# Kernel optimization log

Hardware: AMD Instinct MI355X
Metric: run time of the kernel (lower is better)

Reference implementation:

```python
import jax, jax.numpy as jnp
import numpy as np

LN_EPS = 1e-5

def _layernorm(x, gamma, beta):
    mu = jnp.mean(x, axis=-1, keepdims=True)
    var = jnp.mean(jnp.square(x - mu), axis=-1, keepdims=True)
    return (x - mu) * jax.lax.rsqrt(var + LN_EPS) * gamma + beta

def _gcn_layer(A_hat, H, W, b, g, beta):
    # batched dense-equivalent of per-batch torch.sparse.mm: (B,N,N)@(B,N,F)
    H = jnp.einsum('bnm,bmf->bnf', A_hat, H)
    H = H @ W + b            # Linear
    H = _layernorm(H, g, beta)
    return jax.nn.relu(H)    # dropout is identity in eval

def setup_inputs() -> dict:
    key = jax.random.key(0)
    ks = jax.random.split(key, 8)
    B, N, F, Hd, K, G = 16, 2048, 64, 256, 128, 18
    fuse = Hd + G  # 274
    return {
        'A_hat': jax.random.uniform(ks[0], (B, N, N), dtype=jnp.float32),
        'X': jax.random.normal(ks[1], (B, N, F), dtype=jnp.float32),
        'global_vec': jax.random.normal(ks[2], (B, G), dtype=jnp.float32),
        'W1': jax.random.normal(ks[3], (F, Hd), dtype=jnp.float32) / np.sqrt(F),
        'b1': jnp.zeros((Hd,), jnp.float32),
        'g1': jnp.ones((Hd,), jnp.float32),
        'beta1': jnp.zeros((Hd,), jnp.float32),
        'W2': jax.random.normal(ks[4], (Hd, Hd), dtype=jnp.float32) / np.sqrt(Hd),
        'b2': jnp.zeros((Hd,), jnp.float32),
        'g2': jnp.ones((Hd,), jnp.float32),
        'beta2': jnp.zeros((Hd,), jnp.float32),
        'Ws': jax.random.normal(ks[5], (fuse, 1), dtype=jnp.float32) / np.sqrt(fuse),
        'bs': jnp.zeros((1,), jnp.float32),
        'Wa': jax.random.normal(ks[6], (fuse, K), dtype=jnp.float32) / np.sqrt(fuse),
        'ba': jnp.zeros((K,), jnp.float32),
    }

def reference(A_hat, X, global_vec, W1, b1, g1, beta1, W2, b2, g2, beta2, Ws, bs, Wa, ba):
    H = _gcn_layer(A_hat, X, W1, b1, g1, beta1)
    H = _gcn_layer(A_hat, H, W2, b2, g2, beta2)
    gcnout = jnp.mean(H, axis=1)                       # 'mean' readout -> (B, hidden)
    fused = jnp.concatenate([gcnout, global_vec], axis=-1)  # (B, hidden+18)
    pred_y_reg = (fused @ Ws + bs)[:, 0]               # (B,)
    pred_arr_reg = fused @ Wa + ba                     # (B, K)
    return pred_y_reg, pred_arr_reg
```

## Files before the change

### kernel.cpp

```cpp
#include <hip/hip_runtime.h>

typedef unsigned short u16;
typedef __attribute__((ext_vector_type(8))) short bf16x8;
typedef __attribute__((ext_vector_type(16))) float f32x16;

__device__ __forceinline__ unsigned f2bf(float f) {
  unsigned u = __float_as_uint(f);
  return (u + 0x7fffu + ((u >> 16) & 1u)) >> 16;
}

__device__ __forceinline__ void async16(const u16* g, u16* l) {
  __builtin_amdgcn_global_load_lds(
      (const __attribute__((address_space(1))) void*)g,
      (__attribute__((address_space(3))) void*)l, 16, 0, 0);
}

__global__ __launch_bounds__(256) void prep(
    const float* __restrict__ A, u16* __restrict__ Abf,
    const float* __restrict__ X, u16* __restrict__ Xbf,
    const float* __restrict__ W1, u16* __restrict__ W1T,
    const float* __restrict__ W2, u16* __restrict__ W2T,
    float* __restrict__ GCN)
{
  const long long gid = (long long)blockIdx.x * 256 + threadIdx.x;
  const long long stride = (long long)gridDim.x * 256;
  for (long long i = gid; i < 8388608LL; i += stride) {
    const float4 a = ((const float4*)A)[2 * i];
    const float4 b = ((const float4*)A)[2 * i + 1];
    uint4 r;
    r.x = f2bf(a.x) | (f2bf(a.y) << 16);
    r.y = f2bf(a.z) | (f2bf(a.w) << 16);
    r.z = f2bf(b.x) | (f2bf(b.y) << 16);
    r.w = f2bf(b.z) | (f2bf(b.w) << 16);
    ((uint4*)Abf)[i] = r;
  }
  for (long long i = gid; i < 262144LL; i += stride) {
    const float4 a = ((const float4*)X)[2 * i];
    const float4 b = ((const float4*)X)[2 * i + 1];
    uint4 r;
    r.x = f2bf(a.x) | (f2bf(a.y) << 16);
    r.y = f2bf(a.z) | (f2bf(a.w) << 16);
    r.z = f2bf(b.x) | (f2bf(b.y) << 16);
    r.w = f2bf(b.z) | (f2bf(b.w) << 16);
    ((uint4*)Xbf)[i] = r;
  }
  for (long long i = gid; i < 16384LL; i += stride) {
    const int c = (int)(i >> 6), r = (int)(i & 63);
    W1T[i] = (u16)f2bf(W1[r * 256 + c]);
  }
  for (long long i = gid; i < 65536LL; i += stride) {
    const int c = (int)(i >> 8), r = (int)(i & 255);
    W2T[i] = (u16)f2bf(W2[r * 256 + c]);
  }
  if (gid < 4096) GCN[gid] = 0.f;
}

template<int EPI>
__global__ __launch_bounds__(512, 2) void mm128(
    const u16* __restrict__ Aop, const u16* __restrict__ Bop,
    int K, int lda, int ldb, int ldc,
    long long sA, long long sB, long long sC,
    const float* __restrict__ bias, const float* __restrict__ gam,
    const float* __restrict__ bet, u16* __restrict__ Cb, float* __restrict__ gcn,
    const u16* __restrict__ W2x)
{
  __shared__ __align__(16) u16 As[2][128 * 64];
  __shared__ __align__(16) u16 Bs[2][256 * 64];
  const int tid = threadIdx.x;
  const int w = tid >> 6, lane = tid & 63, l31 = lane & 31, half = lane >> 5;
  const int wm = w >> 2, wn = w & 3;

  const int fid = blockIdx.x + gridDim.x * (blockIdx.y + gridDim.y * blockIdx.z);
  const int pb = gridDim.x * gridDim.y;
  int idx = fid >> 3;
  int bz = fid & 7;
  if (idx >= pb) { bz += 8; idx -= pb; }
  const int m0 = (int)(idx % gridDim.x) * 128;
  const int n0 = (int)(idx / gridDim.x) * 256;

  const int srow = tid >> 3;
  const int clog = (tid & 7) ^ (srow & 7);
  const u16* Ag = Aop + sA * bz + (size_t)(m0 + srow) * lda + clog * 8;
  const u16* Bg = Bop + sB * bz + (size_t)(n0 + srow) * ldb + clog * 8;

  f32x16 acc[2][2];
#pragma unroll
  for (int i = 0; i < 2; i++)
#pragma unroll
    for (int j = 0; j < 2; j++)
#pragma unroll
      for (int r = 0; r < 16; r++) acc[i][j][r] = 0.f;

  const int niter = K >> 6;
  {
    u16* Ad = As[0]; u16* Bd = Bs[0];
    async16(Ag, Ad + tid * 8);
    async16(Ag + (size_t)64 * lda, Ad + 4096 + tid * 8);
#pragma unroll
    for (int p = 0; p < 4; p++)
      async16(Bg + (size_t)(p * 64) * ldb, Bd + p * 4096 + tid * 8);
  }

  for (int i = 0; i < niter; i++) {
    if (i + 1 < niter) {
      const int k1 = (i + 1) << 6;
      u16* Ad = As[(i + 1) & 1]; u16* Bd = Bs[(i + 1) & 1];
      async16(Ag + k1, Ad + tid * 8);
      async16(Ag + (size_t)64 * lda + k1, Ad + 4096 + tid * 8);
#pragma unroll
      for (int p = 0; p < 4; p++)
        async16(Bg + (size_t)(p * 64) * ldb + k1, Bd + p * 4096 + tid * 8);
      __builtin_amdgcn_s_waitcnt(0x0F76);
    } else {
      __builtin_amdgcn_s_waitcnt(0x0F70);
    }
    __builtin_amdgcn_s_barrier();
    __asm__ volatile("" ::: "memory");
    const u16* Ab = As[i & 1];
    const u16* Bb = Bs[i & 1];
#pragma unroll
    for (int kk = 0; kk < 4; kk++) {
      const int pc = ((kk * 2 + half) ^ (l31 & 7)) * 8;
      const bf16x8 a0 = *(const bf16x8*)(Ab + (wm * 64 + l31) * 64 + pc);
      const bf16x8 a1 = *(const bf16x8*)(Ab + (wm * 64 + 32 + l31) * 64 + pc);
      const bf16x8 b0 = *(const bf16x8*)(Bb + (wn * 64 + l31) * 64 + pc);
      const bf16x8 b1 = *(const bf16x8*)(Bb + (wn * 64 + 32 + l31) * 64 + pc);
      acc[0][0] = __builtin_amdgcn_mfma_f32_32x32x16_bf16(a0, b0, acc[0][0], 0, 0, 0);
      acc[0][1] = __builtin_amdgcn_mfma_f32_32x32x16_bf16(a0, b1, acc[0][1], 0, 0, 0);
      acc[1][0] = __builtin_amdgcn_mfma_f32_32x32x16_bf16(a1, b0, acc[1][0], 0, 0, 0);
      acc[1][1] = __builtin_amdgcn_mfma_f32_32x32x16_bf16(a1, b1, acc[1][1], 0, 0, 0);
    }
    __asm__ volatile("" ::: "memory");
    __builtin_amdgcn_s_barrier();
  }

  const int col0 = wn * 64 + l31;

  if constexpr (EPI == 0) {
#pragma unroll
    for (int mt = 0; mt < 2; mt++)
#pragma unroll
      for (int r = 0; r < 16; r++) {
        const int rl = (r & 3) + 8 * (r >> 2) + 4 * half;
        const long long row = (long long)m0 + wm * 64 + mt * 32 + rl;
        Cb[sC * bz + row * ldc + n0 + col0]      = (u16)f2bf(acc[mt][0][r]);
        Cb[sC * bz + row * ldc + n0 + col0 + 32] = (u16)f2bf(acc[mt][1][r]);
      }
    return;
  }

  __syncthreads();
  const float bia0 = bias[col0], bia1 = bias[col0 + 32];
  float s2[2][16];
#pragma unroll
  for (int mt = 0; mt < 2; mt++)
#pragma unroll
    for (int r = 0; r < 16; r++) {
      acc[mt][0][r] += bia0;
      acc[mt][1][r] += bia1;
      s2[mt][r] = acc[mt][0][r] + acc[mt][1][r];
    }
#pragma unroll
  for (int off = 1; off <= 16; off <<= 1)
#pragma unroll
    for (int mt = 0; mt < 2; mt++)
#pragma unroll
      for (int r = 0; r < 16; r++) s2[mt][r] += __shfl_xor(s2[mt][r], off);

  float* sm = (float*)As;
  if (l31 == 0) {
#pragma unroll
    for (int mt = 0; mt < 2; mt++)
#pragma unroll
      for (int r = 0; r < 16; r++) {
        const int rl = (r & 3) + 8 * (r >> 2) + 4 * half;
        sm[wn * 128 + wm * 64 + mt * 32 + rl] = s2[mt][r];
      }
  }
  __syncthreads();
  if (tid < 128)
    sm[512 + tid] = (sm[tid] + sm[128 + tid] + sm[256 + tid] + sm[384 + tid]) * (1.f / 256.f);
  __syncthreads();
  float4 mu4[2][4];
#pragma unroll
  for (int mt = 0; mt < 2; mt++)
#pragma unroll
    for (int g = 0; g < 4; g++)
      mu4[mt][g] = *(const float4*)(sm + 512 + wm * 64 + mt * 32 + g * 8 + 4 * half);

  float q2[2][16];
#pragma unroll
  for (int mt = 0; mt < 2; mt++)
#pragma unroll
    for (int r = 0; r < 16; r++) {
      const float mu = ((const float*)&mu4[mt][r >> 2])[r & 3];
      const float d0 = acc[mt][0][r] - mu, d1 = acc[mt][1][r] - mu;
      q2[mt][r] = d0 * d0 + d1 * d1;
    }
#pragma unroll
  for (int off = 1; off <= 16; off <<= 1)
#pragma unroll
    for (int mt = 0; mt < 2; mt++)
#pragma unroll
      for (int r = 0; r < 16; r++) q2[mt][r] += __shfl_xor(q2[mt][r], off);
  __syncthreads();
  if (l31 == 0) {
#pragma unroll
    for (int mt = 0; mt < 2; mt++)
#pragma unroll
      for (int r = 0; r < 16; r++) {
        const int rl = (r & 3) + 8 * (r >> 2) + 4 * half;
        sm[wn * 128 + wm * 64 + mt * 32 + rl] = q2[mt][r];
      }
  }
  __syncthreads();
  if (tid < 128)
    sm[640 + tid] = rsqrtf(
        (sm[tid] + sm[128 + tid] + sm[256 + tid] + sm[384 + tid]) * (1.f / 256.f) + 1e-5f);
  __syncthreads();
  float4 iv4[2][4];
#pragma unroll
  for (int mt = 0; mt < 2; mt++)
#pragma unroll
    for (int g = 0; g < 4; g++)
      iv4[mt][g] = *(const float4*)(sm + 640 + wm * 64 + mt * 32 + g * 8 + 4 * half);

  const float g0 = gam[col0], g1 = gam[col0 + 32];
  const float e0 = bet[col0], e1 = bet[col0 + 32];
  if constexpr (EPI == 1) {
#pragma unroll
    for (int mt = 0; mt < 2; mt++)
#pragma unroll
      for (int r = 0; r < 16; r++) {
        const float mu = ((const float*)&mu4[mt][r >> 2])[r & 3];
        const float iv = ((const float*)&iv4[mt][r >> 2])[r & 3];
        const int rl = (r & 3) + 8 * (r >> 2) + 4 * half;
        const long long row = (long long)m0 + wm * 64 + mt * 32 + rl;
        const float y0 = fmaxf((acc[mt][0][r] - mu) * iv * g0 + e0, 0.f);
        const float y1 = fmaxf((acc[mt][1][r] - mu) * iv * g1 + e1, 0.f);
        Cb[sC * bz + row * ldc + col0]      = (u16)f2bf(y0);
        Cb[sC * bz + row * ldc + col0 + 32] = (u16)f2bf(y1);
      }
  } else if constexpr (EPI == 2) {
    float c0 = 0.f, c1 = 0.f;
#pragma unroll
    for (int mt = 0; mt < 2; mt++)
#pragma unroll
      for (int r = 0; r < 16; r++) {
        const float mu = ((const float*)&mu4[mt][r >> 2])[r & 3];
        const float iv = ((const float*)&iv4[mt][r >> 2])[r & 3];
        c0 += fmaxf((acc[mt][0][r] - mu) * iv * g0 + e0, 0.f);
        c1 += fmaxf((acc[mt][1][r] - mu) * iv * g1 + e1, 0.f);
      }
    c0 += __shfl_xor(c0, 32);
    c1 += __shfl_xor(c1, 32);
    if (half == 0) {
      atomicAdd(gcn + bz * 256 + col0, c0);
      atomicAdd(gcn + bz * 256 + col0 + 32, c1);
    }
  } else {
    char* H1loc = (char*)Bs;
#pragma unroll
    for (int mt = 0; mt < 2; mt++)
#pragma unroll
      for (int r = 0; r < 16; r++) {
        const float mu = ((const float*)&mu4[mt][r >> 2])[r & 3];
        const float iv = ((const float*)&iv4[mt][r >> 2])[r & 3];
        const int rl = (r & 3) + 8 * (r >> 2) + 4 * half;
        const int row = wm * 64 + mt * 32 + rl;
        const float y0 = fmaxf((acc[mt][0][r] - mu) * iv * g0 + e0, 0.f);
        const float y1 = fmaxf((acc[mt][1][r] - mu) * iv * g1 + e1, 0.f);
        const int xo = (row & 31) << 4;
        *(u16*)(H1loc + row * 512 + ((col0 * 2) ^ xo))        = (u16)f2bf(y0);
        *(u16*)(H1loc + row * 512 + (((col0 + 32) * 2) ^ xo)) = (u16)f2bf(y1);
      }
    __syncthreads();

    u16* Wc = (u16*)As;
    const int orow = (w >> 1) * 64, mcol = (w & 1) * 64;
    const int srw2 = tid >> 2;
    const int cl2 = (tid & 3) ^ (srw2 & 3);

    f32x16 a2[2][2];
#pragma unroll
    for (int i = 0; i < 2; i++)
#pragma unroll
      for (int j = 0; j < 2; j++)
#pragma unroll
        for (int r = 0; r < 16; r++) a2[i][j][r] = 0.f;

#define STAGE_W2(c) do {                                                  \
    u16* _d = Wc + ((c) & 1) * 8192 + tid * 8;                            \
    const u16* _s = W2x + (size_t)srw2 * 256 + (c) * 32 + cl2 * 8;        \
    async16(_s, _d);                                                      \
    async16(_s + 128 * 256, _d + 4096);                                   \
  } while (0)

    STAGE_W2(0);
    STAGE_W2(1);
#pragma unroll
    for (int c = 0; c < 8; c++) {
      if (c < 7) __builtin_amdgcn_s_waitcnt(0x0F72);
      else       __builtin_amdgcn_s_waitcnt(0x0F70);
      __builtin_amdgcn_s_barrier();
      __asm__ volatile("" ::: "memory");
      const u16* bufc = Wc + (c & 1) * 8192;
#pragma unroll
      for (int kk = 0; kk < 2; kk++) {
        const int sl = kk * 2 + half;
        const int ao = (sl ^ (l31 & 3)) * 8;
        const bf16x8 a0 = *(const bf16x8*)(bufc + (orow + l31) * 32 + ao);
        const bf16x8 a1 = *(const bf16x8*)(bufc + (orow + 32 + l31) * 32 + ao);
        const int kb = (c * 32 + sl * 8) * 2;
        const int xo = l31 << 4;
        const bf16x8 b0 = *(const bf16x8*)(H1loc + (mcol + l31) * 512 + (kb ^ xo));
        const bf16x8 b1 = *(const bf16x8*)(H1loc + (mcol + 32 + l31) * 512 + (kb ^ xo));
        a2[0][0] = __builtin_amdgcn_mfma_f32_32x32x16_bf16(a0, b0, a2[0][0], 0, 0, 0);
        a2[0][1] = __builtin_amdgcn_mfma_f32_32x32x16_bf16(a0, b1, a2[0][1], 0, 0, 0);
        a2[1][0] = __builtin_amdgcn_mfma_f32_32x32x16_bf16(a1, b0, a2[1][0], 0, 0, 0);
        a2[1][1] = __builtin_amdgcn_mfma_f32_32x32x16_bf16(a1, b1, a2[1][1], 0, 0, 0);
      }
      __asm__ volatile("" ::: "memory");
      __builtin_amdgcn_s_barrier();
      if (c + 2 < 8) STAGE_W2(c + 2);
    }
#undef STAGE_W2

#pragma unroll
    for (int i = 0; i < 2; i++)
#pragma unroll
      for (int j = 0; j < 2; j++)
#pragma unroll
        for (int r = 0; r < 16; r++) {
          const int rl = (r & 3) + 8 * (r >> 2) + 4 * half;
          const long long rowo = orow + i * 32 + rl;
          const long long colg = m0 + mcol + j * 32 + l31;
          Cb[sC * bz + rowo * ldc + colg] = (u16)f2bf(a2[i][j][r]);
        }
  }
}

__global__ __launch_bounds__(128) void final_kernel(
    const float* __restrict__ gcn, const float* __restrict__ gv,
    const float* __restrict__ Ws, const float* __restrict__ bs,
    const float* __restrict__ Wa, const float* __restrict__ ba,
    float* __restrict__ out)
{
  const int b = blockIdx.x, t = threadIdx.x;
  __shared__ float fused[274];
  fused[t] = gcn[b * 256 + t] * (1.f / 2048.f);
  fused[128 + t] = gcn[b * 256 + 128 + t] * (1.f / 2048.f);
  if (t < 18) fused[256 + t] = gv[b * 18 + t];
  __syncthreads();
  float acc = ba[t];
  for (int i = 0; i < 274; i++) acc = fmaf(fused[i], Wa[i * 128 + t], acc);
  out[16 + b * 128 + t] = acc;
  if (t < 64) {
    float p = 0.f;
    for (int i = t; i < 274; i += 64) p += fused[i] * Ws[i];
#pragma unroll
    for (int off = 32; off >= 1; off >>= 1) p += __shfl_xor(p, off);
    if (t == 0) out[b] = p + bs[0];
  }
}

extern "C" void kernel_launch(void* const* d_in, const int* in_sizes, int n_in,
                              void* d_out, int out_size, void* d_ws, size_t ws_size,
                              hipStream_t stream)
{
  const float* A   = (const float*)d_in[0];
  const float* X   = (const float*)d_in[1];
  const float* GV  = (const float*)d_in[2];
  const float* W1  = (const float*)d_in[3];
  const float* b1  = (const float*)d_in[4];
  const float* g1  = (const float*)d_in[5];
  const float* be1 = (const float*)d_in[6];
  const float* W2  = (const float*)d_in[7];
  const float* b2  = (const float*)d_in[8];
  const float* g2  = (const float*)d_in[9];
  const float* be2 = (const float*)d_in[10];
  const float* Ws  = (const float*)d_in[11];
  const float* bs  = (const float*)d_in[12];
  const float* Wa  = (const float*)d_in[13];
  const float* ba  = (const float*)d_in[14];
  float* out = (float*)d_out;
  (void)in_sizes; (void)n_in; (void)out_size; (void)ws_size;

  char* ws = (char*)d_ws;
  u16*   Abf = (u16*)(ws + 0);
  u16*   Xbf = (u16*)(ws + 134217728);
  u16*   W1T = (u16*)(ws + 138412032);
  u16*   W2T = (u16*)(ws + 138444800);
  u16*   XWT = (u16*)(ws + 138575872);
  u16*   HWT = (u16*)(ws + 155353088);
  float* GCN = (float*)(ws + 172130304);

  prep<<<4096, 256, 0, stream>>>(A, Abf, X, Xbf, W1, W1T, W2, W2T, GCN);

  mm128<0><<<dim3(2, 8, 16), 512, 0, stream>>>(
      W1T, Xbf, 64, 64, 64, 2048, 0LL, 131072LL, 524288LL,
      nullptr, nullptr, nullptr, XWT, nullptr, nullptr);

  mm128<3><<<dim3(16, 1, 16), 512, 0, stream>>>(
      Abf, XWT, 2048, 2048, 2048, 2048, 4194304LL, 524288LL, 524288LL,
      b1, g1, be1, HWT, nullptr, W2T);

  mm128<2><<<dim3(16, 1, 16), 512, 0, stream>>>(
      Abf, HWT, 2048, 2048, 2048, 256, 4194304LL, 524288LL, 524288LL,
      b2, g2, be2, nullptr, GCN, nullptr);

  final_kernel<<<16, 128, 0, stream>>>(GCN, GV, Ws, bs, Wa, ba, out);
}
```

Before: 592.2 us.

## Fuse fp32-to-bf16 conversion of A into the first aggregation GEMM

```diff
diff --git a/kernel.cpp b/kernel.cpp
--- a/kernel.cpp
+++ b/kernel.cpp
@@ -16,7 +16,6 @@
 }
 
 __global__ __launch_bounds__(256) void prep(
-    const float* __restrict__ A, u16* __restrict__ Abf,
     const float* __restrict__ X, u16* __restrict__ Xbf,
     const float* __restrict__ W1, u16* __restrict__ W1T,
     const float* __restrict__ W2, u16* __restrict__ W2T,
@@ -24,16 +23,6 @@
 {
   const long long gid = (long long)blockIdx.x * 256 + threadIdx.x;
   const long long stride = (long long)gridDim.x * 256;
-  for (long long i = gid; i < 8388608LL; i += stride) {
-    const float4 a = ((const float4*)A)[2 * i];
-    const float4 b = ((const float4*)A)[2 * i + 1];
-    uint4 r;
-    r.x = f2bf(a.x) | (f2bf(a.y) << 16);
-    r.y = f2bf(a.z) | (f2bf(a.w) << 16);
-    r.z = f2bf(b.x) | (f2bf(b.y) << 16);
-    r.w = f2bf(b.z) | (f2bf(b.w) << 16);
-    ((uint4*)Abf)[i] = r;
-  }
   for (long long i = gid; i < 262144LL; i += stride) {
     const float4 a = ((const float4*)X)[2 * i];
     const float4 b = ((const float4*)X)[2 * i + 1];
@@ -55,14 +44,15 @@
   if (gid < 4096) GCN[gid] = 0.f;
 }
 
-template<int EPI>
+template<int EPI, int CVTA>
 __global__ __launch_bounds__(512, 2) void mm128(
     const u16* __restrict__ Aop, const u16* __restrict__ Bop,
     int K, int lda, int ldb, int ldc,
     long long sA, long long sB, long long sC,
     const float* __restrict__ bias, const float* __restrict__ gam,
     const float* __restrict__ bet, u16* __restrict__ Cb, float* __restrict__ gcn,
-    const u16* __restrict__ W2x)
+    const u16* __restrict__ W2x, const float* __restrict__ Afp,
+    u16* __restrict__ AbfW)
 {
   __shared__ __align__(16) u16 As[2][128 * 64];
   __shared__ __align__(16) u16 Bs[2][256 * 64];
@@ -83,6 +73,34 @@
   const u16* Ag = Aop + sA * bz + (size_t)(m0 + srow) * lda + clog * 8;
   const u16* Bg = Bop + sB * bz + (size_t)(n0 + srow) * ldb + clog * 8;
 
+  const int ch8 = tid & 7;
+  const float* Af = CVTA ? (Afp + sA * bz + (size_t)(m0 + srow) * lda + ch8 * 8) : nullptr;
+  u16* Aw = CVTA ? (AbfW + sA * bz + (size_t)(m0 + srow) * lda + ch8 * 8) : nullptr;
+  const int dsoff = srow * 64 + ((ch8 ^ (srow & 7)) * 8);
+
+  float4 a4[4];
+#define LOAD_A4(k) do {                                                   \
+    a4[0] = *(const float4*)(Af + (k));                                   \
+    a4[1] = *(const float4*)(Af + (k) + 4);                               \
+    a4[2] = *(const float4*)(Af + (size_t)64 * lda + (k));                \
+    a4[3] = *(const float4*)(Af + (size_t)64 * lda + (k) + 4);            \
+  } while (0)
+#define CVT_WRITE(dst, k) do {                                            \
+    uint4 r0, r1;                                                         \
+    r0.x = f2bf(a4[0].x) | (f2bf(a4[0].y) << 16);                         \
+    r0.y = f2bf(a4[0].z) | (f2bf(a4[0].w) << 16);                         \
+    r0.z = f2bf(a4[1].x) | (f2bf(a4[1].y) << 16);                         \
+    r0.w = f2bf(a4[1].z) | (f2bf(a4[1].w) << 16);                         \
+    r1.x = f2bf(a4[2].x) | (f2bf(a4[2].y) << 16);                         \
+    r1.y = f2bf(a4[2].z) | (f2bf(a4[2].w) << 16);                         \
+    r1.z = f2bf(a4[3].x) | (f2bf(a4[3].y) << 16);                         \
+    r1.w = f2bf(a4[3].z) | (f2bf(a4[3].w) << 16);                         \
+    *(uint4*)((dst) + dsoff)        = r0;                                 \
+    *(uint4*)((dst) + 4096 + dsoff) = r1;                                 \
+    *(uint4*)(Aw + (k))                      = r0;                        \
+    *(uint4*)(Aw + (size_t)64 * lda + (k))   = r1;                        \
+  } while (0)
+
   f32x16 acc[2][2];
 #pragma unroll
   for (int i = 0; i < 2; i++)
@@ -92,7 +110,14 @@
       for (int r = 0; r < 16; r++) acc[i][j][r] = 0.f;
 
   const int niter = K >> 6;
-  {
+  if constexpr (CVTA) {
+    LOAD_A4(0);
+#pragma unroll
+    for (int p = 0; p < 4; p++)
+      async16(Bg + (size_t)(p * 64) * ldb, Bs[0] + p * 4096 + tid * 8);
+    __builtin_amdgcn_s_waitcnt(0x0F74);
+    CVT_WRITE(As[0], 0);
+  } else {
     u16* Ad = As[0]; u16* Bd = Bs[0];
     async16(Ag, Ad + tid * 8);
     async16(Ag + (size_t)64 * lda, Ad + 4096 + tid * 8);
@@ -102,17 +127,30 @@
   }
 
   for (int i = 0; i < niter; i++) {
-    if (i + 1 < niter) {
-      const int k1 = (i + 1) << 6;
-      u16* Ad = As[(i + 1) & 1]; u16* Bd = Bs[(i + 1) & 1];
-      async16(Ag + k1, Ad + tid * 8);
-      async16(Ag + (size_t)64 * lda + k1, Ad + 4096 + tid * 8);
-#pragma unroll
-      for (int p = 0; p < 4; p++)
-        async16(Bg + (size_t)(p * 64) * ldb + k1, Bd + p * 4096 + tid * 8);
-      __builtin_amdgcn_s_waitcnt(0x0F76);
+    const int k1 = (i + 1) << 6;
+    if constexpr (CVTA) {
+      if (i + 1 < niter) {
+        LOAD_A4(k1);
+        u16* Bd = Bs[(i + 1) & 1];
+#pragma unroll
+        for (int p = 0; p < 4; p++)
+          async16(Bg + (size_t)(p * 64) * ldb + k1, Bd + p * 4096 + tid * 8);
+        __builtin_amdgcn_s_waitcnt(0x007A);
+      } else {
+        __builtin_amdgcn_s_waitcnt(0x0072);
+      }
     } else {
-      __builtin_amdgcn_s_waitcnt(0x0F70);
+      if (i + 1 < niter) {
+        u16* Ad = As[(i + 1) & 1]; u16* Bd = Bs[(i + 1) & 1];
+        async16(Ag + k1, Ad + tid * 8);
+        async16(Ag + (size_t)64 * lda + k1, Ad + 4096 + tid * 8);
+#pragma unroll
+        for (int p = 0; p < 4; p++)
+          async16(Bg + (size_t)(p * 64) * ldb + k1, Bd + p * 4096 + tid * 8);
+        __builtin_amdgcn_s_waitcnt(0x0F76);
+      } else {
+        __builtin_amdgcn_s_waitcnt(0x0F70);
+      }
     }
     __builtin_amdgcn_s_barrier();
     __asm__ volatile("" ::: "memory");
@@ -130,9 +168,17 @@
       acc[1][0] = __builtin_amdgcn_mfma_f32_32x32x16_bf16(a1, b0, acc[1][0], 0, 0, 0);
       acc[1][1] = __builtin_amdgcn_mfma_f32_32x32x16_bf16(a1, b1, acc[1][1], 0, 0, 0);
     }
+    if constexpr (CVTA) {
+      if (i + 1 < niter) {
+        __builtin_amdgcn_s_waitcnt(0x0F74);
+        CVT_WRITE(As[(i + 1) & 1], k1);
+      }
+    }
     __asm__ volatile("" ::: "memory");
     __builtin_amdgcn_s_barrier();
   }
+#undef LOAD_A4
+#undef CVT_WRITE
 
   const int col0 = wn * 64 + l31;
 
@@ -227,21 +273,7 @@
 
   const float g0 = gam[col0], g1 = gam[col0 + 32];
   const float e0 = bet[col0], e1 = bet[col0 + 32];
-  if constexpr (EPI == 1) {
-#pragma unroll
-    for (int mt = 0; mt < 2; mt++)
-#pragma unroll
-      for (int r = 0; r < 16; r++) {
-        const float mu = ((const float*)&mu4[mt][r >> 2])[r & 3];
-        const float iv = ((const float*)&iv4[mt][r >> 2])[r & 3];
-        const int rl = (r & 3) + 8 * (r >> 2) + 4 * half;
-        const long long row = (long long)m0 + wm * 64 + mt * 32 + rl;
-        const float y0 = fmaxf((acc[mt][0][r] - mu) * iv * g0 + e0, 0.f);
-        const float y1 = fmaxf((acc[mt][1][r] - mu) * iv * g1 + e1, 0.f);
-        Cb[sC * bz + row * ldc + col0]      = (u16)f2bf(y0);
-        Cb[sC * bz + row * ldc + col0 + 32] = (u16)f2bf(y1);
-      }
-  } else if constexpr (EPI == 2) {
+  if constexpr (EPI == 2) {
     float c0 = 0.f, c1 = 0.f;
 #pragma unroll
     for (int mt = 0; mt < 2; mt++)
@@ -395,19 +427,19 @@
   u16*   HWT = (u16*)(ws + 155353088);
   float* GCN = (float*)(ws + 172130304);
 
-  prep<<<4096, 256, 0, stream>>>(A, Abf, X, Xbf, W1, W1T, W2, W2T, GCN);
-
-  mm128<0><<<dim3(2, 8, 16), 512, 0, stream>>>(
+  prep<<<512, 256, 0, stream>>>(X, Xbf, W1, W1T, W2, W2T, GCN);
+
+  mm128<0, 0><<<dim3(2, 8, 16), 512, 0, stream>>>(
       W1T, Xbf, 64, 64, 64, 2048, 0LL, 131072LL, 524288LL,
-      nullptr, nullptr, nullptr, XWT, nullptr, nullptr);
-
-  mm128<3><<<dim3(16, 1, 16), 512, 0, stream>>>(
+      nullptr, nullptr, nullptr, XWT, nullptr, nullptr, nullptr, nullptr);
+
+  mm128<3, 1><<<dim3(16, 1, 16), 512, 0, stream>>>(
       Abf, XWT, 2048, 2048, 2048, 2048, 4194304LL, 524288LL, 524288LL,
-      b1, g1, be1, HWT, nullptr, W2T);
-
-  mm128<2><<<dim3(16, 1, 16), 512, 0, stream>>>(
+      b1, g1, be1, HWT, nullptr, W2T, A, Abf);
+
+  mm128<2, 0><<<dim3(16, 1, 16), 512, 0, stream>>>(
       Abf, HWT, 2048, 2048, 2048, 256, 4194304LL, 524288LL, 524288LL,
-      b2, g2, be2, nullptr, GCN, nullptr);
+      b2, g2, be2, nullptr, GCN, nullptr, nullptr, nullptr);
 
   final_kernel<<<16, 128, 0, stream>>>(GCN, GV, Ws, bs, Wa, ba, out);
 }
```

Result: faster. 568.1 us (-4.1%).
